# Optimization experiments

Measured on AMD Instinct MI355X. Metric: run time of the kernel, lower is better.

Reference implementation:

```python
import jax, jax.numpy as jnp
import numpy as np
from jax.scipy.special import logsumexp

C = 1024   # num HMM states
H = 256    # hidden_dim
V = 10000  # vocab size
B = 16     # batch
N = 256    # sequence length
EPS = 1e-5


def _layernorm(x, g, b):
    mu = x.mean(-1, keepdims=True)
    var = ((x - mu) ** 2).mean(-1, keepdims=True)
    return g * (x - mu) * jax.lax.rsqrt(var + EPS) + b


def _residual(x, W1, b1, W2, b2, g, beta):
    # ResidualLayer: ln(relu(lin2(relu(lin1(x)))) + relu(lin1(x))), dropout=0
    h = jax.nn.relu(x @ W1.T + b1)
    return _layernorm(jax.nn.relu(h @ W2.T + b2) + h, g, beta)


def setup_inputs() -> dict:
    key = jax.random.key(0)
    ks = iter(jax.random.split(key, 40))
    def nrm(shape, scale):
        return jax.random.normal(next(ks), shape, dtype=jnp.float32) * scale
    w = 1.0 / np.sqrt(H)
    inp = {}
    # embeddings (torch.randn)
    inp['start_emb'] = nrm((C, H), 1.0)
    inp['state_emb'] = nrm((C, H), 1.0)
    inp['pre_emb'] = nrm((C, H), 1.0)
    # start_mlp: ResidualLayer(H,H) + Linear(H,1)
    for p, out_dim in (('s', 1), ('t', C), ('e', V)):
        inp[p + '_W1'] = nrm((H, H), w)
        inp[p + '_b1'] = jnp.zeros((H,), jnp.float32)
        inp[p + '_W2'] = nrm((H, H), w)
        inp[p + '_b2'] = jnp.zeros((H,), jnp.float32)
        inp[p + '_g'] = jnp.ones((H,), jnp.float32)
        inp[p + '_beta'] = jnp.zeros((H,), jnp.float32)
        inp[p + '_Wo'] = nrm((out_dim, H), w)
        inp[p + '_bo'] = jnp.zeros((out_dim,), jnp.float32)
    inp['text'] = jax.random.randint(next(ks), (B, N), 0, V)
    return inp


def reference(start_emb, state_emb, pre_emb,
              s_W1, s_b1, s_W2, s_b2, s_g, s_beta, s_Wo, s_bo,
              t_W1, t_b1, t_W2, t_b2, t_g, t_beta, t_Wo, t_bo,
              e_W1, e_b1, e_W2, e_b2, e_g, e_beta, e_Wo, e_bo,
              text):
    # start: (C,) log init distribution
    start = jax.nn.log_softmax(
        (_residual(start_emb, s_W1, s_b1, s_W2, s_b2, s_g, s_beta) @ s_Wo.T + s_bo).squeeze(-1))
    # transition[i, j] = log p(z_t = j | z_{t-1} = i), shape (C, C)
    transition = jax.nn.log_softmax(
        _residual(state_emb, t_W1, t_b1, t_W2, t_b2, t_g, t_beta) @ t_Wo.T + t_bo, axis=-1)
    # emission[c, v] = log p(x = v | z = c), shape (C, V)
    emission = jax.nn.log_softmax(
        _residual(pre_emb, e_W1, e_b1, e_W2, e_b2, e_g, e_beta) @ e_Wo.T + e_bo, axis=-1)

    emit = emission.T[text]              # (B, N, C): log p(x_t | z_t = c)
    alpha0 = start[None, :] + emit[:, 0]  # (B, C)

    def step(alpha, e_t):
        # log-semiring matmul: alpha_next[b,j] = lse_i(alpha[b,i] + T[i,j]) + emit
        a = logsumexp(alpha[:, :, None] + transition[None], axis=1) + e_t
        return a, None

    alphaT, _ = jax.lax.scan(step, alpha0, jnp.swapaxes(emit[:, 1:], 0, 1))
    return logsumexp(alphaT, axis=-1).sum()
```

## Files before the change

### kernel.cpp

```cpp
#include <hip/hip_runtime.h>
#include <hip/hip_bf16.h>

typedef __attribute__((ext_vector_type(8))) short short8;
typedef __attribute__((ext_vector_type(4))) float f32x4;
typedef unsigned short ushort;
typedef unsigned long long u64;
typedef unsigned int u32;

#define AL(p) __hip_atomic_load((p), __ATOMIC_RELAXED, __HIP_MEMORY_SCOPE_AGENT)
#define AS(p,v) __hip_atomic_store((p), (v), __ATOMIC_RELAXED, __HIP_MEMORY_SCOPE_AGENT)

__device__ inline ushort f2bf(float x) {
  __hip_bfloat16 h = __float2bfloat16(x);
  return *reinterpret_cast<ushort*>(&h);
}
__device__ inline float bfhi2f(u32 lo) {
  union { u32 u; float f; } c; c.u = lo & 0xFFFF0000u; return c.f;
}
__device__ inline float bflo2f(u32 lo) {
  union { u32 u; float f; } c; c.u = lo << 16; return c.f;
}
__device__ inline u32 pk2(float a, float b) {
  return (u32)f2bf(__expf(a)) | ((u32)f2bf(__expf(b)) << 16);
}

__global__ __launch_bounds__(256) void mlp3_kernel(
    const float* X0, const float* W10, const float* b10, const float* W20, const float* b20,
    const float* g0, const float* be0, float* of0, ushort* ob0,
    const float* X1, const float* W11, const float* b11, const float* W21, const float* b21,
    const float* g1, const float* be1, float* of1, ushort* ob1,
    const float* X2, const float* W12, const float* b12, const float* W22, const float* b22,
    const float* g2, const float* be2, float* of2, ushort* ob2,
    const float* ca_i, ushort* ca_o, int nc_a,
    const float* cb_i, ushort* cb_o, int nc_b)
{
  int y = blockIdx.y;
  if (y == 3) {
    int i = blockIdx.x * 256 + threadIdx.x;
    int st = 64 * 256;
    for (; i < nc_a + nc_b; i += st) {
      if (i < nc_a) ca_o[i] = f2bf(ca_i[i]);
      else          cb_o[i - nc_a] = f2bf(cb_i[i - nc_a]);
    }
    return;
  }
  const float *X, *W1, *b1, *W2, *b2, *g, *beta; float* of32; ushort* obf;
  if (y == 0)      { X=X0; W1=W10; b1=b10; W2=W20; b2=b20; g=g0; beta=be0; of32=of0; obf=ob0; }
  else if (y == 1) { X=X1; W1=W11; b1=b11; W2=W21; b2=b21; g=g1; beta=be1; of32=of1; obf=ob1; }
  else             { X=X2; W1=W12; b1=b12; W2=W22; b2=b22; g=g2; beta=be2; of32=of2; obf=ob2; }

  __shared__ float Xs[16 * 260];
  __shared__ float H1s[16 * 260];
  __shared__ float mu_s[16], rs_s[16];
  int tid = threadIdx.x;
  int r0 = blockIdx.x * 16;
  for (int q = 0; q < 16; ++q) Xs[q * 260 + tid] = X[(r0 + q) * 256 + tid];
  __syncthreads();
  int r = tid & 15, jg = tid >> 4;
  for (int jj = 0; jj < 16; ++jj) {
    int j = jg * 16 + jj;
    const float4* wrow = (const float4*)(W1 + j * 256);
    const float4* xrow = (const float4*)(Xs + r * 260);
    float acc = 0.f;
#pragma unroll 8
    for (int kq = 0; kq < 64; ++kq) {
      float4 w = wrow[kq], x = xrow[kq];
      acc += w.x * x.x + w.y * x.y + w.z * x.z + w.w * x.w;
    }
    acc += b1[j];
    H1s[r * 260 + j] = acc > 0.f ? acc : 0.f;
  }
  __syncthreads();
  for (int jj = 0; jj < 16; ++jj) {
    int j = jg * 16 + jj;
    const float4* wrow = (const float4*)(W2 + j * 256);
    const float4* hrow = (const float4*)(H1s + r * 260);
    float acc = 0.f;
#pragma unroll 8
    for (int kq = 0; kq < 64; ++kq) {
      float4 w = wrow[kq], x = hrow[kq];
      acc += w.x * x.x + w.y * x.y + w.z * x.z + w.w * x.w;
    }
    acc += b2[j];
    float v = (acc > 0.f ? acc : 0.f) + H1s[r * 260 + j];
    Xs[r * 260 + j] = v;
  }
  __syncthreads();
  if (tid < 16) {
    float s = 0.f, s2 = 0.f;
    for (int k = 0; k < 256; ++k) { float x = Xs[tid * 260 + k]; s += x; s2 += x * x; }
    float mu = s * (1.0f / 256.0f);
    float var = s2 * (1.0f / 256.0f) - mu * mu;
    mu_s[tid] = mu; rs_s[tid] = rsqrtf(var + 1e-5f);
  }
  __syncthreads();
  for (int q = 0; q < 16; ++q) {
    float x = (Xs[q * 260 + tid] - mu_s[q]) * rs_s[q] * g[tid] + beta[tid];
    if (of32) of32[(r0 + q) * 256 + tid] = x;
    if (obf)  obf[(r0 + q) * 256 + tid] = f2bf(x);
  }
}

__device__ void shead_body(const float* __restrict__ h, const float* __restrict__ Wo,
                           const float* __restrict__ bo, float* __restrict__ start)
{
  __shared__ float red[4];
  __shared__ float lse_s;
  int tid = threadIdx.x;
  float lg[4];
  float s = 0.f;
#pragma unroll
  for (int q = 0; q < 4; ++q) {
    int state = q * 256 + tid;
    const float4* wr = (const float4*)Wo;
    const float4* hr = (const float4*)(h + state * 256);
    float acc = 0.f;
    for (int kq = 0; kq < 64; ++kq) {
      float4 w = wr[kq], x = hr[kq];
      acc += w.x * x.x + w.y * x.y + w.z * x.z + w.w * x.w;
    }
    acc += bo[0];
    lg[q] = acc;
    s += __expf(acc);
  }
  for (int m = 1; m < 64; m <<= 1) s += __shfl_xor(s, m);
  if ((tid & 63) == 0) red[tid >> 6] = s;
  __syncthreads();
  if (tid == 0) lse_s = logf(red[0] + red[1] + red[2] + red[3]);
  __syncthreads();
  float lse = lse_s;
#pragma unroll
  for (int q = 0; q < 4; ++q) start[q * 256 + tid] = lg[q] - lse;
}

__device__ void gemm_body(const ushort* __restrict__ A, const ushort* __restrict__ Bw,
                          int mode, int Nvalid, int chunks,
                          const float* __restrict__ bias,
                          float* __restrict__ out, float* __restrict__ esum,
                          const int* __restrict__ text, int bx, int by)
{
  __shared__ ushort As[64 * 264];
  __shared__ ushort Bs[32 * 264];
  int tid = threadIdx.x;
  int m0 = bx * 64;
#pragma unroll
  for (int q = 0; q < 8; ++q) {
    int idx = q * 256 + tid;
    int row = idx >> 5, c8 = idx & 31;
    *(short8*)(As + row * 264 + c8 * 8) = *(const short8*)(A + (m0 + row) * 256 + c8 * 8);
  }
  int lane = tid & 63, wave = tid >> 6;
  int r16 = lane & 15, quad = lane >> 4;
  float sacc[4] = {0.f, 0.f, 0.f, 0.f};

  for (int c = 0; c < chunks; ++c) {
    int n0 = (by * chunks + c) * 32;
    if (c) __syncthreads();
#pragma unroll
    for (int q = 0; q < 4; ++q) {
      int idx = q * 256 + tid;
      int row = idx >> 5, c8 = idx & 31;
      int grow = n0 + row;
      short8 val = {0, 0, 0, 0, 0, 0, 0, 0};
      if (mode == 2) {
        int v = text[(grow & 15) * 256 + (grow >> 4)];
        val = *(const short8*)(Bw + v * 256 + c8 * 8);
      } else if (grow < Nvalid) {
        val = *(const short8*)(Bw + grow * 256 + c8 * 8);
      }
      *(short8*)(Bs + row * 264 + c8 * 8) = val;
    }
    __syncthreads();
    f32x4 acc0 = {0.f, 0.f, 0.f, 0.f}, acc1 = {0.f, 0.f, 0.f, 0.f};
#pragma unroll
    for (int kb = 0; kb < 8; ++kb) {
      short8 a  = *(const short8*)(As + (wave * 16 + r16) * 264 + kb * 32 + quad * 8);
      short8 b0 = *(const short8*)(Bs + r16 * 264 + kb * 32 + quad * 8);
      short8 b1 = *(const short8*)(Bs + (16 + r16) * 264 + kb * 32 + quad * 8);
      acc0 = __builtin_amdgcn_mfma_f32_16x16x32_bf16(a, b0, acc0, 0, 0, 0);
      acc1 = __builtin_amdgcn_mfma_f32_16x16x32_bf16(a, b1, acc1, 0, 0, 0);
    }
    if (mode == 0) {
#pragma unroll
      for (int rr = 0; rr < 4; ++rr) {
        int row = m0 + wave * 16 + quad * 4 + rr;
        int c0 = n0 + r16, c1 = n0 + 16 + r16;
        out[row * 1024 + c0] = acc0[rr] + bias[c0];
        out[row * 1024 + c1] = acc1[rr] + bias[c1];
      }
    } else if (mode == 1) {
#pragma unroll
      for (int rr = 0; rr < 4; ++rr) {
        int c0 = n0 + r16, c1 = n0 + 16 + r16;
        float p0 = (c0 < Nvalid) ? __expf(acc0[rr] + bias[c0]) : 0.f;
        float p1 = (c1 < Nvalid) ? __expf(acc1[rr] + bias[c1]) : 0.f;
        sacc[rr] += p0 + p1;
      }
    } else {
      int c0 = m0 + wave * 16 + quad * 4;
      int tb0 = n0 + r16, tb1 = n0 + 16 + r16;
      int v0 = text[(tb0 & 15) * 256 + (tb0 >> 4)];
      int v1 = text[(tb1 & 15) * 256 + (tb1 >> 4)];
      float l0 = logf(esum[c0]), l1 = logf(esum[c0 + 1]);
      float l2 = logf(esum[c0 + 2]), l3 = logf(esum[c0 + 3]);
      float4 o0, o1;
      o0.x = acc0[0] + bias[v0] - l0; o0.y = acc0[1] + bias[v0] - l1;
      o0.z = acc0[2] + bias[v0] - l2; o0.w = acc0[3] + bias[v0] - l3;
      o1.x = acc1[0] + bias[v1] - l0; o1.y = acc1[1] + bias[v1] - l1;
      o1.z = acc1[2] + bias[v1] - l2; o1.w = acc1[3] + bias[v1] - l3;
      *(float4*)(out + tb0 * 1024 + c0) = o0;
      *(float4*)(out + tb1 * 1024 + c0) = o1;
    }
  }
  if (mode == 1) {
#pragma unroll
    for (int rr = 0; rr < 4; ++rr) {
      float s = sacc[rr];
      s += __shfl_xor(s, 1); s += __shfl_xor(s, 2);
      s += __shfl_xor(s, 4); s += __shfl_xor(s, 8);
      if (r16 == 0) atomicAdd(esum + m0 + wave * 16 + quad * 4 + rr, s);
    }
  }
}

__device__ void trans_body(const float* __restrict__ logits, ushort* __restrict__ texp_frag,
                           int i)
{
  __shared__ float red[4];
  __shared__ float lse_s;
  int tid = threadIdx.x;
  float x[4];
  float s = 0.f;
#pragma unroll
  for (int q = 0; q < 4; ++q) { x[q] = logits[i * 1024 + q * 256 + tid]; s += __expf(x[q]); }
  for (int m = 1; m < 64; m <<= 1) s += __shfl_xor(s, m);
  if ((tid & 63) == 0) red[tid >> 6] = s;
  __syncthreads();
  if (tid == 0) lse_s = logf(red[0] + red[1] + red[2] + red[3]);
  __syncthreads();
  float lse = lse_s;
  int kblk = i >> 5, quad = (i >> 3) & 3, idx = i & 7;
#pragma unroll
  for (int q = 0; q < 4; ++q) {
    int j = q * 256 + tid;
    int pos = (((j >> 4) * 32 + kblk) * 64 + quad * 16 + (j & 15)) * 8 + idx;
    texp_frag[pos] = f2bf(__expf(x[q] - lse));
  }
}

__global__ __launch_bounds__(256) void g01s_kernel(
    const ushort* At, const ushort* Bt, const float* t_bo, float* tlogits,
    const ushort* Ae, const ushort* Be, const float* e_bo, float* esum,
    const float* h_s, const float* s_Wo, const float* s_bo, float* start_v)
{
  int p = blockIdx.x;
  if (p < 512) {
    gemm_body(At, Bt, 0, 1024, 1, t_bo, tlogits, nullptr, nullptr, p & 15, p >> 4);
  } else if (p < 1152) {
    int q = p - 512;
    gemm_body(Ae, Be, 1, 10000, 8, e_bo, nullptr, esum, nullptr, q & 15, q >> 4);
  } else {
    shead_body(h_s, s_Wo, s_bo, start_v);
  }
}

__global__ __launch_bounds__(256) void tg2_kernel(
    const float* tlogits, ushort* texp_frag,
    const ushort* Ae, const ushort* Be, const float* e_bo, float* emitg,
    float* esum, const int* text)
{
  int p = blockIdx.x;
  if (p < 1024) {
    trans_body(tlogits, texp_frag, p);
  } else {
    int q = p - 1024;
    gemm_body(Ae, Be, 2, 4096, 1, e_bo, emitg, esum, text, q & 15, q >> 4);
  }
}

__global__ __launch_bounds__(256, 1) void scan_kernel(
    const ushort* __restrict__ texp_frag,
    const float* __restrict__ emitg,
    const float* __restrict__ start_v,
    u64* __restrict__ abuf,
    float* __restrict__ out)
{
  __shared__ __align__(16) char Asb[2][4 * 2080];
  __shared__ float redw[4][4], reds[4][4];

  int tid = threadIdx.x, lane = tid & 63, wave = tid >> 6;
  int r16 = lane & 15, quad = lane >> 4;
  int p = blockIdx.x, bg = p & 3, cb = p >> 2;
  int b0 = bg * 4;

  const short8* tg = (const short8*)texp_frag + (size_t)cb * 8192 + wave * 2048;
  short8 treg[32];
#pragma unroll
  for (int k = 0; k < 32; ++k) treg[k] = tg[k * 64 + lane];
#pragma unroll
  for (int k = 0; k < 32; ++k) asm volatile("" : "+a"(treg[k]));

  int colw = cb * 64 + wave * 16 + r16;
  int abase = (r16 & 3) * 2080 + quad * 16;

  float m_r[4], Bs[4];
#pragma unroll
  for (int i = 0; i < 4; ++i) {
    m_r[i] = start_v[0] + emitg[(size_t)(b0 + i) * 1024];
    Bs[i] = m_r[i];
  }
  {
    int c0 = 2 * tid, c2 = 2 * tid + 512;
    char* ab = Asb[1];
#pragma unroll
    for (int r = 0; r < 4; ++r) {
      const float* eb = emitg + (size_t)(b0 + r) * 1024;
      float v0 = start_v[c0] + eb[c0],     v1 = start_v[c0 + 1] + eb[c0 + 1];
      float v2 = start_v[c2] + eb[c2],     v3 = start_v[c2 + 1] + eb[c2 + 1];
      *(u32*)(ab + r * 2080 + 4 * tid)        = pk2(v0 - m_r[r], v1 - m_r[r]);
      *(u32*)(ab + r * 2080 + 1024 + 4 * tid) = pk2(v2 - m_r[r], v3 - m_r[r]);
    }
  }
  __syncthreads();

  for (int t = 1; t < 256; ++t) {
    float e0 = 0.f, e1 = 0.f, e2 = 0.f, e3 = 0.f;
    if (quad == 0) {
      const float* ep = emitg + (size_t)(t * 16 + b0) * 1024 + colw;
      e0 = ep[0]; e1 = ep[1024]; e2 = ep[2048]; e3 = ep[3072];
    }

    const char* ab = Asb[t & 1];
    f32x4 a0, a1, a2, a3;
    {
      short8 f0 = *(const short8*)(ab + abase);
      short8 f1 = *(const short8*)(ab + abase + 64);
      short8 f2 = *(const short8*)(ab + abase + 128);
      short8 f3 = *(const short8*)(ab + abase + 192);
      asm volatile("v_mfma_f32_16x16x32_bf16 %0, %1, %2, 0" : "=v"(a0) : "v"(f0), "a"(treg[0]));
      asm volatile("v_mfma_f32_16x16x32_bf16 %0, %1, %2, 0" : "=v"(a1) : "v"(f1), "a"(treg[1]));
      asm volatile("v_mfma_f32_16x16x32_bf16 %0, %1, %2, 0" : "=v"(a2) : "v"(f2), "a"(treg[2]));
      asm volatile("v_mfma_f32_16x16x32_bf16 %0, %1, %2, 0" : "=v"(a3) : "v"(f3), "a"(treg[3]));
    }
#pragma unroll
    for (int kb = 4; kb < 32; kb += 4) {
      short8 f0 = *(const short8*)(ab + abase + kb * 64);
      short8 f1 = *(const short8*)(ab + abase + kb * 64 + 64);
      short8 f2 = *(const short8*)(ab + abase + kb * 64 + 128);
      short8 f3 = *(const short8*)(ab + abase + kb * 64 + 192);
      asm volatile("v_mfma_f32_16x16x32_bf16 %0, %1, %2, %0" : "+v"(a0) : "v"(f0), "a"(treg[kb + 0]));
      asm volatile("v_mfma_f32_16x16x32_bf16 %0, %1, %2, %0" : "+v"(a1) : "v"(f1), "a"(treg[kb + 1]));
      asm volatile("v_mfma_f32_16x16x32_bf16 %0, %1, %2, %0" : "+v"(a2) : "v"(f2), "a"(treg[kb + 2]));
      asm volatile("v_mfma_f32_16x16x32_bf16 %0, %1, %2, %0" : "+v"(a3) : "v"(f3), "a"(treg[kb + 3]));
    }
    asm volatile("s_nop 7\n\ts_nop 7\n\ts_nop 1"
                 : "+v"(a0), "+v"(a1), "+v"(a2), "+v"(a3));
    f32x4 acc = (a0 + a1) + (a2 + a3);

    if (quad == 0) {
      float d0 = __logf(acc[0]) + e0;
      float d1 = __logf(acc[1]) + e1;
      float d2 = __logf(acc[2]) + e2;
      float d3 = __logf(acc[3]) + e3;
      u64 tag = ((u64)(u32)t) << 32;
      u64* ob = abuf + (t & 1) * 8192 + bg * 2048 + colw;
      AS(ob,        tag | (u64)((u32)f2bf(d0) | ((u32)f2bf(d1) << 16)));
      AS(ob + 1024, tag | (u64)((u32)f2bf(d2) | ((u32)f2bf(d3) << 16)));
    }

    if (t < 255) {
      u64 x0, x1, x2, x3, x4, x5, x6, x7, n0, n1;
      {
        const u64* buf = abuf + (t & 1) * 8192 + bg * 2048;
        int oa = 2 * tid, oc = 2 * tid + 512;
        u32 want = (u32)t;
        bool first = true;
        for (;;) {
          if (!first) __builtin_amdgcn_s_sleep(1);
          first = false;
          x0 = AL(buf + oa);        x1 = AL(buf + oa + 1);
          x2 = AL(buf + oc);        x3 = AL(buf + oc + 1);
          x4 = AL(buf + 1024 + oa); x5 = AL(buf + 1024 + oa + 1);
          x6 = AL(buf + 1024 + oc); x7 = AL(buf + 1024 + oc + 1);
          n0 = AL(buf);             n1 = AL(buf + 1024);
          u32 bad = ((u32)(x0 >> 32) ^ want) | ((u32)(x1 >> 32) ^ want) |
                    ((u32)(x2 >> 32) ^ want) | ((u32)(x3 >> 32) ^ want) |
                    ((u32)(x4 >> 32) ^ want) | ((u32)(x5 >> 32) ^ want) |
                    ((u32)(x6 >> 32) ^ want) | ((u32)(x7 >> 32) ^ want) |
                    ((u32)(n0 >> 32) ^ want) | ((u32)(n1 >> 32) ^ want);
          if (bad == 0) break;
        }
      }
      m_r[0] = bflo2f((u32)n0); m_r[1] = bfhi2f((u32)n0);
      m_r[2] = bflo2f((u32)n1); m_r[3] = bfhi2f((u32)n1);
      Bs[0] += m_r[0]; Bs[1] += m_r[1]; Bs[2] += m_r[2]; Bs[3] += m_r[3];

      char* aw = Asb[(t + 1) & 1];
      u32 l0 = (u32)x0, l1 = (u32)x1, l2 = (u32)x2, l3 = (u32)x3;
      u32 l4 = (u32)x4, l5 = (u32)x5, l6 = (u32)x6, l7 = (u32)x7;
      *(u32*)(aw + 4 * tid)                = pk2(bflo2f(l0) - m_r[0], bflo2f(l1) - m_r[0]);
      *(u32*)(aw + 1024 + 4 * tid)         = pk2(bflo2f(l2) - m_r[0], bflo2f(l3) - m_r[0]);
      *(u32*)(aw + 2080 + 4 * tid)         = pk2(bfhi2f(l0) - m_r[1], bfhi2f(l1) - m_r[1]);
      *(u32*)(aw + 2080 + 1024 + 4 * tid)  = pk2(bfhi2f(l2) - m_r[1], bfhi2f(l3) - m_r[1]);
      *(u32*)(aw + 4160 + 4 * tid)         = pk2(bflo2f(l4) - m_r[2], bflo2f(l5) - m_r[2]);
      *(u32*)(aw + 4160 + 1024 + 4 * tid)  = pk2(bflo2f(l6) - m_r[2], bflo2f(l7) - m_r[2]);
      *(u32*)(aw + 6240 + 4 * tid)         = pk2(bfhi2f(l4) - m_r[3], bfhi2f(l5) - m_r[3]);
      *(u32*)(aw + 6240 + 1024 + 4 * tid)  = pk2(bfhi2f(l6) - m_r[3], bfhi2f(l7) - m_r[3]);
      __syncthreads();
    }
  }

  if (cb == 0) {
    const u64* fb = abuf + 8192 + bg * 2048;
    int oa = 2 * tid, oc = 2 * tid + 512;
    u64 x0, x1, x2, x3, x4, x5, x6, x7;
    {
      bool first = true;
      for (;;) {
        if (!first) __builtin_amdgcn_s_sleep(1);
        first = false;
        x0 = AL(fb + oa);        x1 = AL(fb + oa + 1);
        x2 = AL(fb + oc);        x3 = AL(fb + oc + 1);
        x4 = AL(fb + 1024 + oa); x5 = AL(fb + 1024 + oa + 1);
        x6 = AL(fb + 1024 + oc); x7 = AL(fb + 1024 + oc + 1);
        u32 bad = ((u32)(x0 >> 32) ^ 255u) | ((u32)(x1 >> 32) ^ 255u) |
                  ((u32)(x2 >> 32) ^ 255u) | ((u32)(x3 >> 32) ^ 255u) |
                  ((u32)(x4 >> 32) ^ 255u) | ((u32)(x5 >> 32) ^ 255u) |
                  ((u32)(x6 >> 32) ^ 255u) | ((u32)(x7 >> 32) ^ 255u);
        if (bad == 0) break;
      }
    }
    float bv[4][4];
    bv[0][0] = bflo2f((u32)x0); bv[0][1] = bflo2f((u32)x1); bv[0][2] = bflo2f((u32)x2); bv[0][3] = bflo2f((u32)x3);
    bv[1][0] = bfhi2f((u32)x0); bv[1][1] = bfhi2f((u32)x1); bv[1][2] = bfhi2f((u32)x2); bv[1][3] = bfhi2f((u32)x3);
    bv[2][0] = bflo2f((u32)x4); bv[2][1] = bflo2f((u32)x5); bv[2][2] = bflo2f((u32)x6); bv[2][3] = bflo2f((u32)x7);
    bv[3][0] = bfhi2f((u32)x4); bv[3][1] = bfhi2f((u32)x5); bv[3][2] = bfhi2f((u32)x6); bv[3][3] = bfhi2f((u32)x7);
    float M[4], S[4];
#pragma unroll
    for (int i = 0; i < 4; ++i)
      M[i] = fmaxf(fmaxf(bv[i][0], bv[i][1]), fmaxf(bv[i][2], bv[i][3]));
    for (int off = 1; off < 64; off <<= 1) {
#pragma unroll
      for (int i = 0; i < 4; ++i) M[i] = fmaxf(M[i], __shfl_xor(M[i], off));
    }
    if (lane == 0) { redw[wave][0]=M[0]; redw[wave][1]=M[1]; redw[wave][2]=M[2]; redw[wave][3]=M[3]; }
    __syncthreads();
#pragma unroll
    for (int i = 0; i < 4; ++i)
      M[i] = fmaxf(fmaxf(redw[0][i], redw[1][i]), fmaxf(redw[2][i], redw[3][i]));
#pragma unroll
    for (int i = 0; i < 4; ++i)
      S[i] = __expf(bv[i][0] - M[i]) + __expf(bv[i][1] - M[i]) +
             __expf(bv[i][2] - M[i]) + __expf(bv[i][3] - M[i]);
    for (int off = 1; off < 64; off <<= 1) {
#pragma unroll
      for (int i = 0; i < 4; ++i) S[i] += __shfl_xor(S[i], off);
    }
    if (lane == 0) { reds[wave][0]=S[0]; reds[wave][1]=S[1]; reds[wave][2]=S[2]; reds[wave][3]=S[3]; }
    __syncthreads();
    if (tid == 0) {
      float tot = 0.f;
#pragma unroll
      for (int i = 0; i < 4; ++i) {
        float Sg = reds[0][i] + reds[1][i] + reds[2][i] + reds[3][i];
        tot += Bs[i] + M[i] + logf(Sg);
      }
      atomicAdd(out, tot);
    }
  }
}

extern "C" void kernel_launch(void* const* d_in, const int* in_sizes, int n_in,
                              void* d_out, int out_size, void* d_ws, size_t ws_size,
                              hipStream_t stream)
{
  (void)in_sizes; (void)n_in; (void)out_size; (void)ws_size;
  const float* start_emb = (const float*)d_in[0];
  const float* state_emb = (const float*)d_in[1];
  const float* pre_emb   = (const float*)d_in[2];
  const float* s_W1 = (const float*)d_in[3];  const float* s_b1 = (const float*)d_in[4];
  const float* s_W2 = (const float*)d_in[5];  const float* s_b2 = (const float*)d_in[6];
  const float* s_g  = (const float*)d_in[7];  const float* s_be = (const float*)d_in[8];
  const float* s_Wo = (const float*)d_in[9];  const float* s_bo = (const float*)d_in[10];
  const float* t_W1 = (const float*)d_in[11]; const float* t_b1 = (const float*)d_in[12];
  const float* t_W2 = (const float*)d_in[13]; const float* t_b2 = (const float*)d_in[14];
  const float* t_g  = (const float*)d_in[15]; const float* t_be = (const float*)d_in[16];
  const float* t_Wo = (const float*)d_in[17]; const float* t_bo = (const float*)d_in[18];
  const float* e_W1 = (const float*)d_in[19]; const float* e_b1 = (const float*)d_in[20];
  const float* e_W2 = (const float*)d_in[21]; const float* e_b2 = (const float*)d_in[22];
  const float* e_g  = (const float*)d_in[23]; const float* e_be = (const float*)d_in[24];
  const float* e_Wo = (const float*)d_in[25]; const float* e_bo = (const float*)d_in[26];
  const int*   text = (const int*)d_in[27];
  float* out = (float*)d_out;

  char* ws = (char*)d_ws;
  size_t off = 0;
  auto alloc = [&](size_t bytes) -> char* {
    char* p = ws + off;
    off = (off + bytes + 255) & ~(size_t)255;
    return p;
  };
  float* esum       = (float*)alloc(1024 * 4);
  u64*   abuf       = (u64*)alloc(2 * 8192 * 8);
  float* start_v    = (float*)alloc(1024 * 4);
  float* h_s        = (float*)alloc(1024 * 256 * 4);
  ushort* h_t_bf    = (ushort*)alloc(1024 * 256 * 2);
  ushort* h_e_bf    = (ushort*)alloc(1024 * 256 * 2);
  ushort* tWo_bf    = (ushort*)alloc(1024 * 256 * 2);
  ushort* eWo_bf    = (ushort*)alloc(10000 * 256 * 2);
  float* tlogits    = (float*)alloc(1024 * 1024 * 4);
  ushort* texp_frag = (ushort*)alloc(1024 * 1024 * 2);
  float* emitg      = (float*)alloc(4096 * 1024 * 4);

  hipMemsetAsync(ws, 0, 4096 + 2 * 8192 * 8, stream);
  hipMemsetAsync(d_out, 0, 4, stream);

  mlp3_kernel<<<dim3(64, 4), 256, 0, stream>>>(
      start_emb, s_W1, s_b1, s_W2, s_b2, s_g, s_be, h_s, nullptr,
      state_emb, t_W1, t_b1, t_W2, t_b2, t_g, t_be, nullptr, h_t_bf,
      pre_emb,  e_W1, e_b1, e_W2, e_b2, e_g, e_be, nullptr, h_e_bf,
      t_Wo, tWo_bf, 1024 * 256, e_Wo, eWo_bf, 10000 * 256);

  g01s_kernel<<<1153, 256, 0, stream>>>(
      h_t_bf, tWo_bf, t_bo, tlogits,
      h_e_bf, eWo_bf, e_bo, esum,
      h_s, s_Wo, s_bo, start_v);

  tg2_kernel<<<3072, 256, 0, stream>>>(
      tlogits, texp_frag,
      h_e_bf, eWo_bf, e_bo, emitg,
      esum, text);

  scan_kernel<<<64, 256, 0, stream>>>(texp_frag, emitg, start_v, abuf, out);
}
```

Measured before the change: 881.1 us.

## Fuse transition/emission producer kernel with scan using per-timestep readiness counters

Merges the transition-exp and emission-gather GEMM kernel with the HMM forward scan into one launch. The first 64 blocks run the scan and spin on atomic counters until the transition fragments and each pair of timesteps' emission rows are published. The remaining blocks produce the data and bump the counters with release semantics. The goal is to overlap the serial scan with emission production and remove a kernel boundary. It depends on the 64 scan blocks being scheduled and on producer blocks making progress while the scan blocks spin, which risks deadlock or contention if the scan blocks occupy CUs the producers need.

Result: slower. 1.207 ms (+37.0%).

```diff
diff --git a/kernel.cpp b/kernel.cpp
--- a/kernel.cpp
+++ b/kernel.cpp
@@ -9,6 +9,7 @@
 
 #define AL(p) __hip_atomic_load((p), __ATOMIC_RELAXED, __HIP_MEMORY_SCOPE_AGENT)
 #define AS(p,v) __hip_atomic_store((p), (v), __ATOMIC_RELAXED, __HIP_MEMORY_SCOPE_AGENT)
+#define ALQ(p) __hip_atomic_load((p), __ATOMIC_ACQUIRE, __HIP_MEMORY_SCOPE_AGENT)
 
 __device__ inline ushort f2bf(float x) {
   __hip_bfloat16 h = __float2bfloat16(x);
@@ -264,34 +265,42 @@
   }
 }
 
-__global__ __launch_bounds__(256) void tg2_kernel(
-    const float* tlogits, ushort* texp_frag,
-    const ushort* Ae, const ushort* Be, const float* e_bo, float* emitg,
-    float* esum, const int* text)
-{
-  int p = blockIdx.x;
-  if (p < 1024) {
-    trans_body(tlogits, texp_frag, p);
-  } else {
-    int q = p - 1024;
-    gemm_body(Ae, Be, 2, 4096, 1, e_bo, emitg, esum, text, q & 15, q >> 4);
-  }
-}
-
-__global__ __launch_bounds__(256, 1) void scan_kernel(
-    const ushort* __restrict__ texp_frag,
-    const float* __restrict__ emitg,
+__global__ __launch_bounds__(256, 1) void tgscan_kernel(
+    const float* __restrict__ tlogits, ushort* __restrict__ texp_frag,
+    const ushort* __restrict__ Ae, const ushort* __restrict__ Be,
+    const float* __restrict__ e_bo, float* __restrict__ emitg,
+    float* __restrict__ esum, const int* __restrict__ text,
     const float* __restrict__ start_v,
     u64* __restrict__ abuf,
-    float* __restrict__ out)
-{
+    float* __restrict__ out,
+    u32* __restrict__ cnt)
+{
+  int p = blockIdx.x;
+  if (p >= 64) {
+    if (p < 1088) {
+      trans_body(tlogits, texp_frag, p - 64);
+      __syncthreads();
+      if (threadIdx.x == 0)
+        __hip_atomic_fetch_add(cnt, 1u, __ATOMIC_RELEASE, __HIP_MEMORY_SCOPE_AGENT);
+    } else {
+      int q = p - 1088;
+      gemm_body(Ae, Be, 2, 4096, 1, e_bo, emitg, esum, text, q & 15, q >> 4);
+      __syncthreads();
+      if (threadIdx.x == 0)
+        __hip_atomic_fetch_add(cnt + 1 + (q >> 4), 1u, __ATOMIC_RELEASE, __HIP_MEMORY_SCOPE_AGENT);
+    }
+    return;
+  }
+
   __shared__ __align__(16) char Asb[2][4 * 2080];
   __shared__ float redw[4][4], reds[4][4];
 
   int tid = threadIdx.x, lane = tid & 63, wave = tid >> 6;
   int r16 = lane & 15, quad = lane >> 4;
-  int p = blockIdx.x, bg = p & 3, cb = p >> 2;
+  int bg = p & 3, cb = p >> 2;
   int b0 = bg * 4;
+
+  while (ALQ(cnt) < 1024u) __builtin_amdgcn_s_sleep(8);
 
   const short8* tg = (const short8*)texp_frag + (size_t)cb * 8192 + wave * 2048;
   short8 treg[32];
@@ -302,6 +311,8 @@
 
   int colw = cb * 64 + wave * 16 + r16;
   int abase = (r16 & 3) * 2080 + quad * 16;
+
+  while (ALQ(cnt + 1) < 16u) __builtin_amdgcn_s_sleep(8);
 
   float m_r[4], Bs[4];
 #pragma unroll
@@ -324,6 +335,10 @@
   __syncthreads();
 
   for (int t = 1; t < 256; ++t) {
+    if ((t & 1) == 0) {
+      const u32* ct = cnt + 1 + (t >> 1);
+      while (ALQ(ct) < 16u) __builtin_amdgcn_s_sleep(2);
+    }
     float e0 = 0.f, e1 = 0.f, e2 = 0.f, e3 = 0.f;
     if (quad == 0) {
       const float* ep = emitg + (size_t)(t * 16 + b0) * 1024 + colw;
@@ -502,6 +517,7 @@
   };
   float* esum       = (float*)alloc(1024 * 4);
   u64*   abuf       = (u64*)alloc(2 * 8192 * 8);
+  u32*   cnt        = (u32*)alloc(256 * 4);
   float* start_v    = (float*)alloc(1024 * 4);
   float* h_s        = (float*)alloc(1024 * 256 * 4);
   ushort* h_t_bf    = (ushort*)alloc(1024 * 256 * 2);
@@ -512,7 +528,7 @@
   ushort* texp_frag = (ushort*)alloc(1024 * 1024 * 2);
   float* emitg      = (float*)alloc(4096 * 1024 * 4);
 
-  hipMemsetAsync(ws, 0, 4096 + 2 * 8192 * 8, stream);
+  hipMemsetAsync(ws, 0, 4096 + 2 * 8192 * 8 + 1024, stream);
   hipMemsetAsync(d_out, 0, 4, stream);
 
   mlp3_kernel<<<dim3(64, 4), 256, 0, stream>>>(
@@ -526,10 +542,8 @@
       h_e_bf, eWo_bf, e_bo, esum,
       h_s, s_Wo, s_bo, start_v);
 
-  tg2_kernel<<<3072, 256, 0, stream>>>(
+  tgscan_kernel<<<3136, 256, 0, stream>>>(
       tlogits, texp_frag,
       h_e_bf, eWo_bf, e_bo, emitg,
-      esum, text);
-
-  scan_kernel<<<64, 256, 0, stream>>>(texp_frag, emitg, start_v, abuf, out);
-}
+      esum, text, start_v, abuf, out, cnt);
+}
```
